# Performance work log

Measured on AMD Instinct MI355X. Metric: run time of the kernel, lower is better.

The kernel has to match this reference:

```python
import jax, jax.numpy as jnp
import numpy as np

# Stochastic-computing layer: values in [0,1] are encoded as random bitstreams
# (bit = uniform <= value), multiply = AND, and the reduction over input rows is
# a chained random MUX (tf.where with p=0.5 coins), then mean over the bit axis.
BATCH, D_IN, D_OUT, BIT_SIZE = 512, 1024, 1024, 128


def setup_inputs() -> dict:
    key = jax.random.key(0)
    kx, kw = jax.random.split(key)
    # bitstream-encoded probabilities in [0, 1]
    x = jax.random.uniform(kx, (BATCH, D_IN), dtype=jnp.float32)
    w = jax.random.uniform(kw, (D_IN, D_OUT), dtype=jnp.float32)
    return {"x": x, "w": w}


def reference(x, w):
    B, Din = x.shape
    Dout = w.shape[1]
    key = jax.random.key(42)
    kx, kw, kc = jax.random.split(key, 3)

    # bitstream generation: bit = (uniform <= value)
    x_bits = jax.random.uniform(kx, (B, Din, BIT_SIZE)) <= x[:, :, None]        # (B, Din, T) bool
    w_bits = jax.random.uniform(kw, (Din, Dout, BIT_SIZE)) <= w[:, :, None]     # (Din, Dout, T) bool

    # Chained random MUX over rows 1..Din-2 (mirrors `for row in range(1, dim-1)`):
    #   final = where(coin, final, row_r)  ->  result is row r of the LAST step
    #   whose coin was False; row 0 if every coin was True. Coins are shared
    #   across the output dim (original select_line shape (B, 1, T)).
    n_steps = Din - 2
    coins = jax.random.uniform(kc, (n_steps, B, BIT_SIZE)) <= 0.5               # (steps, B, T) bool
    rows = jnp.arange(1, Din - 1)                                               # (steps,)
    idx = jnp.max(jnp.where(~coins, rows[:, None, None], 0), axis=0)            # (B, T) int

    # Gather the selected row's bits instead of materializing (B, Din, Dout, T)
    chosen_x = jnp.take_along_axis(x_bits, idx[:, None, :], axis=1)[:, 0, :]    # (B, T)
    w_bt = jnp.transpose(w_bits, (0, 2, 1))                                     # (Din, T, Dout)
    chosen_w = w_bt[idx, jnp.arange(BIT_SIZE)[None, :], :]                      # (B, T, Dout)

    # stochastic multiply (AND) then decode via mean over the bit axis
    final = (chosen_x[:, :, None] & chosen_w).astype(jnp.float32)               # (B, T, Dout)
    return jnp.mean(final, axis=1)                                              # (B, Dout)
```

## Files before the change

kernel.cpp:

```cpp
#include <hip/hip_runtime.h>
#include <stdint.h>

#define BATCH 512
#define D_IN 1024
#define D_OUT 1024
#define BITSZ 128
#define N_STEPS (D_IN - 2)

#define IBASE 960
#define ICAP 64

#define WS_V_OFF 0u
#define WS_V_BYTES (BATCH * BITSZ * 4u)
#define WS_TAB_OFF (WS_V_OFF + WS_V_BYTES)
#define WS_TAB_BYTES (BITSZ * ICAP * 32u * 4u)
#define WS_NEEDED (WS_TAB_OFF + WS_TAB_BYTES)

#define MCAP 128
#define TSTRIDE 132

__host__ __device__ __forceinline__ uint32_t rotl32(uint32_t x, uint32_t d) {
  return (x << d) | (x >> (32u - d));
}

__host__ __device__ __forceinline__ void threefry2x32(uint32_t k0, uint32_t k1,
                                                      uint32_t& x0, uint32_t& x1) {
  const uint32_t k2 = k0 ^ k1 ^ 0x1BD11BDAu;
  x0 += k0; x1 += k1;
#define TFR(r) { x0 += x1; x1 = rotl32(x1, (r)); x1 ^= x0; }
  TFR(13) TFR(15) TFR(26) TFR(6)
  x0 += k1; x1 += k2 + 1u;
  TFR(17) TFR(29) TFR(16) TFR(24)
  x0 += k2; x1 += k0 + 2u;
  TFR(13) TFR(15) TFR(26) TFR(6)
  x0 += k0; x1 += k1 + 3u;
  TFR(17) TFR(29) TFR(16) TFR(24)
  x0 += k1; x1 += k2 + 4u;
  TFR(13) TFR(15) TFR(26) TFR(6)
  x0 += k2; x1 += k0 + 5u;
#undef TFR
}

__device__ __forceinline__ float runif(uint32_t k0, uint32_t k1, uint32_t n) {
  uint32_t x0 = 0u, x1 = n;
  threefry2x32(k0, k1, x0, x1);
  const uint32_t b = x0 ^ x1;
  return __uint_as_float((b >> 9) | 0x3f800000u) - 1.0f;
}

__global__ void __launch_bounds__(256) k_idx(const float* __restrict__ x,
                                             int* __restrict__ v,
                                             uint32_t ck0, uint32_t ck1,
                                             uint32_t xk0, uint32_t xk1) {
  const int tid = blockIdx.x * 256 + threadIdx.x;
  const int b = tid >> 7;
  const int t = tid & 127;

  int idx = 0;
  int s;
  for (s = N_STEPS - 1; s >= 3; s -= 4) {
    const float u0 = runif(ck0, ck1, ((uint32_t)(s)     << 16) + (uint32_t)tid);
    const float u1 = runif(ck0, ck1, ((uint32_t)(s - 1) << 16) + (uint32_t)tid);
    const float u2 = runif(ck0, ck1, ((uint32_t)(s - 2) << 16) + (uint32_t)tid);
    const float u3 = runif(ck0, ck1, ((uint32_t)(s - 3) << 16) + (uint32_t)tid);
    if (u0 > 0.5f) { idx = s + 1; break; }
    if (u1 > 0.5f) { idx = s;     break; }
    if (u2 > 0.5f) { idx = s - 1; break; }
    if (u3 > 0.5f) { idx = s - 2; break; }
  }
  if (idx == 0 && s < 3) {
    const float u0 = runif(ck0, ck1, (1u << 16) + (uint32_t)tid);
    const float u1 = runif(ck0, ck1, (uint32_t)tid);
    if (u0 > 0.5f)      idx = 2;
    else if (u1 > 0.5f) idx = 1;
  }

  const float ux = runif(xk0, xk1,
      ((uint32_t)b << 17) + ((uint32_t)idx << 7) + (uint32_t)t);
  const int xb = (ux <= x[b * D_IN + idx]) ? 1 : 0;
  v[tid] = xb ? idx : -1;
}

__global__ void __launch_bounds__(256) k_tab(const float* __restrict__ w,
                                             const int* __restrict__ v,
                                             uint32_t* __restrict__ tab,
                                             uint32_t wk0, uint32_t wk1) {
  const int t = blockIdx.x >> 2;
  const int q = blockIdx.x & 3;
  const int tid = threadIdx.x;

  __shared__ uint32_t s_bm[2];
  if (tid < 2) s_bm[tid] = 0u;
  __syncthreads();

  unsigned long long m64 = 0;
  {
    const int v0 = v[tid * BITSZ + t];
    const int v1 = v[(tid + 256) * BITSZ + t];
    if (v0 >= IBASE) m64 |= 1ull << (v0 - IBASE);
    if (v1 >= IBASE) m64 |= 1ull << (v1 - IBASE);
  }
  for (int off = 32; off; off >>= 1) m64 |= __shfl_down(m64, off);
  if ((tid & 63) == 0) {
    atomicOr(&s_bm[0], (uint32_t)m64);
    atomicOr(&s_bm[1], (uint32_t)(m64 >> 32));
  }
  __syncthreads();

  unsigned long long bm = (unsigned long long)s_bm[0] |
                          ((unsigned long long)s_bm[1] << 32);
  const int d = q * 256 + tid;
  const int lane = tid & 63;
  const int wbase = (d >> 5) & ~1;
  while (bm) {
    const int j = __builtin_ctzll(bm);
    bm &= bm - 1ull;
    const int i = IBASE + j;
    const float u = runif(wk0, wk1,
        ((uint32_t)i << 17) + ((uint32_t)d << 7) + (uint32_t)t);
    const unsigned long long mb = __ballot(u <= w[i * D_OUT + d]);
    uint32_t* row = tab + (((t << 6) + j) << 5);
    if (lane == 0)  row[wbase]     = (uint32_t)mb;
    if (lane == 32) row[wbase + 1] = (uint32_t)(mb >> 32);
  }
}

__global__ void __launch_bounds__(1024) k_acc(const float* __restrict__ w,
                                              const int* __restrict__ v,
                                              const uint32_t* __restrict__ tab,
                                              float* __restrict__ out,
                                              uint32_t wk0, uint32_t wk1,
                                              int use_tab) {
  const int b = blockIdx.x;
  const int tid = threadIdx.x;

  __shared__ __align__(16) uint32_t s_tab2[32 * TSTRIDE];
  __shared__ int s_list[BITSZ];
  __shared__ int s_wcnt[2];
  __shared__ int s_anyfb;

  if (tid == 0) s_anyfb = use_tab ? 0 : 1;
  __syncthreads();

  unsigned long long mb = 0;
  int code = -1;
  bool act = false;
  if (tid < BITSZ) {
    code = v[b * BITSZ + tid];
    act = code >= 0;
    mb = __ballot(act);
    if ((tid & 63) == 0) s_wcnt[tid >> 6] = __popcll(mb);
  }
  __syncthreads();
  const int m = s_wcnt[0] + s_wcnt[1];
  const int m4 = (m + 3) & ~3;
  if (tid < BITSZ && act) {
    const int lane = tid & 63;
    const int pos = ((tid >= 64) ? s_wcnt[0] : 0) +
                    __popcll(mb & ((1ull << lane) - 1ull));
    s_list[pos] = (code << 7) | tid;
    if (code < IBASE) atomicOr(&s_anyfb, 1);
  }
  __syncthreads();

  if (s_anyfb == 0) {
    const int wrd = tid & 31;
    for (int jj = tid >> 5; jj < m; jj += 32) {
      const int e = s_list[jj];
      const int i = e >> 7, t = e & 127;
      s_tab2[wrd * TSTRIDE + jj] = tab[(((t << 6) + (i - IBASE)) << 5) + wrd];
    }
    if (tid < 32)
      for (int jj = m; jj < m4; ++jj) s_tab2[tid * TSTRIDE + jj] = 0u;
    __syncthreads();

    const int dw = tid >> 5, db = tid & 31;
    const uint32_t* colp = &s_tab2[dw * TSTRIDE];
    int acc = 0;
    for (int k = 0; k < m4; k += 4) {
      const uint4 r = *(const uint4*)(colp + k);
      acc += (r.x >> db) & 1u;
      acc += (r.y >> db) & 1u;
      acc += (r.z >> db) & 1u;
      acc += (r.w >> db) & 1u;
    }
    out[b * D_OUT + tid] = (float)acc * (1.0f / (float)BITSZ);
  } else {
    int acc = 0;
    for (int jj = 0; jj < m; ++jj) {
      const int e = s_list[jj];
      const int i = e >> 7, t = e & 127;
      const float u = runif(wk0, wk1,
          ((uint32_t)i << 17) + ((uint32_t)tid << 7) + (uint32_t)t);
      acc += (u <= w[i * D_OUT + tid]) ? 1 : 0;
    }
    out[b * D_OUT + tid] = (float)acc * (1.0f / (float)BITSZ);
  }
}

struct TFKeys { uint32_t xk0, xk1, wk0, wk1, ck0, ck1; };

static TFKeys derive_keys() {
  TFKeys K;
  uint32_t a0 = 0, a1 = 0; threefry2x32(0u, 42u, a0, a1); K.xk0 = a0; K.xk1 = a1;
  uint32_t b0 = 0, b1 = 1; threefry2x32(0u, 42u, b0, b1); K.wk0 = b0; K.wk1 = b1;
  uint32_t c0 = 0, c1 = 2; threefry2x32(0u, 42u, c0, c1); K.ck0 = c0; K.ck1 = c1;
  return K;
}

extern "C" void kernel_launch(void* const* d_in, const int* in_sizes, int n_in,
                              void* d_out, int out_size, void* d_ws, size_t ws_size,
                              hipStream_t stream) {
  const float* x = (const float*)d_in[0];
  const float* w = (const float*)d_in[1];
  if (n_in >= 2 && in_sizes[0] == D_IN * D_OUT && in_sizes[1] == BATCH * D_IN) {
    const float* tmp = x; x = w; w = tmp;
  }
  float* out = (float*)d_out;
  char* ws = (char*)d_ws;
  int* v = (int*)(ws + WS_V_OFF);
  uint32_t* tab = (uint32_t*)(ws + WS_TAB_OFF);

  const int use_tab = (ws_size >= WS_NEEDED) ? 1 : 0;
  const TFKeys K = derive_keys();

  hipLaunchKernelGGL(k_idx, dim3((BATCH * BITSZ) / 256), dim3(256), 0, stream,
                     x, v, K.ck0, K.ck1, K.xk0, K.xk1);
  if (use_tab)
    hipLaunchKernelGGL(k_tab, dim3(BITSZ * 4), dim3(256), 0, stream,
                       w, v, tab, K.wk0, K.wk1);
  hipLaunchKernelGGL(k_acc, dim3(BATCH), dim3(D_OUT), 0, stream,
                     w, v, tab, out, K.wk0, K.wk1, use_tab);
}
```

Baseline: 22.47 us.

## Fuse index scan into table-building kernel to drop one launch

Merges the index-selection kernel and the w-bit table kernel into one. Each of the four output-quarter blocks for a bit position recomputes the coin scan for all 512 batch rows, and only quarter 0 writes v. This removes a kernel launch and the global round trip of v between them, at the cost of doing the Threefry scan work four times. A __syncthreads in k_acc after initialising s_anyfb is also removed; this looks safe because a later barrier comes before the atomicOr on s_anyfb.

```diff
diff --git a/kernel.cpp b/kernel.cpp
--- a/kernel.cpp
+++ b/kernel.cpp
@@ -16,7 +16,6 @@
 #define WS_TAB_BYTES (BITSZ * ICAP * 32u * 4u)
 #define WS_NEEDED (WS_TAB_OFF + WS_TAB_BYTES)
 
-#define MCAP 128
 #define TSTRIDE 132
 
 __host__ __device__ __forceinline__ uint32_t rotl32(uint32_t x, uint32_t d) {
@@ -48,6 +47,79 @@
   return __uint_as_float((b >> 9) | 0x3f800000u) - 1.0f;
 }
 
+__device__ __forceinline__ int scan_idx(int b, int t,
+                                        uint32_t ck0, uint32_t ck1) {
+  const uint32_t bt = ((uint32_t)b << 7) + (uint32_t)t;
+  int idx = 0;
+  int s;
+  for (s = N_STEPS - 1; s >= 3; s -= 4) {
+    const float u0 = runif(ck0, ck1, ((uint32_t)(s)     << 16) + bt);
+    const float u1 = runif(ck0, ck1, ((uint32_t)(s - 1) << 16) + bt);
+    const float u2 = runif(ck0, ck1, ((uint32_t)(s - 2) << 16) + bt);
+    const float u3 = runif(ck0, ck1, ((uint32_t)(s - 3) << 16) + bt);
+    if (u0 > 0.5f) { idx = s + 1; break; }
+    if (u1 > 0.5f) { idx = s;     break; }
+    if (u2 > 0.5f) { idx = s - 1; break; }
+    if (u3 > 0.5f) { idx = s - 2; break; }
+  }
+  if (idx == 0 && s < 3) {
+    const float u0 = runif(ck0, ck1, (1u << 16) + bt);
+    const float u1 = runif(ck0, ck1, bt);
+    if (u0 > 0.5f)      idx = 2;
+    else if (u1 > 0.5f) idx = 1;
+  }
+  return idx;
+}
+
+__global__ void __launch_bounds__(256) k_tabx(const float* __restrict__ x,
+                                              const float* __restrict__ w,
+                                              int* __restrict__ v,
+                                              uint32_t* __restrict__ tab,
+                                              uint32_t ck0, uint32_t ck1,
+                                              uint32_t xk0, uint32_t xk1,
+                                              uint32_t wk0, uint32_t wk1) {
+  const int t = blockIdx.x & 127;
+  const int q = blockIdx.x >> 7;
+  const int tid = threadIdx.x;
+
+  __shared__ uint32_t s_bm[2];
+  if (tid < 2) s_bm[tid] = 0u;
+  __syncthreads();
+
+#pragma unroll
+  for (int h = 0; h < 2; ++h) {
+    const int b = tid + h * 256;
+    const int idx = scan_idx(b, t, ck0, ck1);
+    const float ux = runif(xk0, xk1,
+        ((uint32_t)b << 17) + ((uint32_t)idx << 7) + (uint32_t)t);
+    const int xb = (ux <= x[b * D_IN + idx]) ? 1 : 0;
+    if (q == 0) v[b * BITSZ + t] = xb ? idx : -1;
+    if (xb && idx >= IBASE) {
+      const int bp = idx - IBASE;
+      atomicOr(&s_bm[bp >> 5], 1u << (bp & 31));
+    }
+  }
+  __syncthreads();
+
+  unsigned long long bm = (unsigned long long)s_bm[0] |
+                          ((unsigned long long)s_bm[1] << 32);
+  const int d = q * 256 + tid;
+  const int lane = tid & 63;
+  const int wbase = (d >> 5) & ~1;
+  const float* wcol = w + d;
+  while (bm) {
+    const int j = __builtin_ctzll(bm);
+    bm &= bm - 1ull;
+    const int i = IBASE + j;
+    const float u = runif(wk0, wk1,
+        ((uint32_t)i << 17) + ((uint32_t)d << 7) + (uint32_t)t);
+    const unsigned long long mb = __ballot(u <= wcol[i * D_OUT]);
+    uint32_t* row = tab + (((t << 6) + j) << 5);
+    if (lane == 0)  row[wbase]     = (uint32_t)mb;
+    if (lane == 32) row[wbase + 1] = (uint32_t)(mb >> 32);
+  }
+}
+
 __global__ void __launch_bounds__(256) k_idx(const float* __restrict__ x,
                                              int* __restrict__ v,
                                              uint32_t ck0, uint32_t ck1,
@@ -55,74 +127,11 @@
   const int tid = blockIdx.x * 256 + threadIdx.x;
   const int b = tid >> 7;
   const int t = tid & 127;
-
-  int idx = 0;
-  int s;
-  for (s = N_STEPS - 1; s >= 3; s -= 4) {
-    const float u0 = runif(ck0, ck1, ((uint32_t)(s)     << 16) + (uint32_t)tid);
-    const float u1 = runif(ck0, ck1, ((uint32_t)(s - 1) << 16) + (uint32_t)tid);
-    const float u2 = runif(ck0, ck1, ((uint32_t)(s - 2) << 16) + (uint32_t)tid);
-    const float u3 = runif(ck0, ck1, ((uint32_t)(s - 3) << 16) + (uint32_t)tid);
-    if (u0 > 0.5f) { idx = s + 1; break; }
-    if (u1 > 0.5f) { idx = s;     break; }
-    if (u2 > 0.5f) { idx = s - 1; break; }
-    if (u3 > 0.5f) { idx = s - 2; break; }
-  }
-  if (idx == 0 && s < 3) {
-    const float u0 = runif(ck0, ck1, (1u << 16) + (uint32_t)tid);
-    const float u1 = runif(ck0, ck1, (uint32_t)tid);
-    if (u0 > 0.5f)      idx = 2;
-    else if (u1 > 0.5f) idx = 1;
-  }
-
+  const int idx = scan_idx(b, t, ck0, ck1);
   const float ux = runif(xk0, xk1,
       ((uint32_t)b << 17) + ((uint32_t)idx << 7) + (uint32_t)t);
   const int xb = (ux <= x[b * D_IN + idx]) ? 1 : 0;
   v[tid] = xb ? idx : -1;
-}
-
-__global__ void __launch_bounds__(256) k_tab(const float* __restrict__ w,
-                                             const int* __restrict__ v,
-                                             uint32_t* __restrict__ tab,
-                                             uint32_t wk0, uint32_t wk1) {
-  const int t = blockIdx.x >> 2;
-  const int q = blockIdx.x & 3;
-  const int tid = threadIdx.x;
-
-  __shared__ uint32_t s_bm[2];
-  if (tid < 2) s_bm[tid] = 0u;
-  __syncthreads();
-
-  unsigned long long m64 = 0;
-  {
-    const int v0 = v[tid * BITSZ + t];
-    const int v1 = v[(tid + 256) * BITSZ + t];
-    if (v0 >= IBASE) m64 |= 1ull << (v0 - IBASE);
-    if (v1 >= IBASE) m64 |= 1ull << (v1 - IBASE);
-  }
-  for (int off = 32; off; off >>= 1) m64 |= __shfl_down(m64, off);
-  if ((tid & 63) == 0) {
-    atomicOr(&s_bm[0], (uint32_t)m64);
-    atomicOr(&s_bm[1], (uint32_t)(m64 >> 32));
-  }
-  __syncthreads();
-
-  unsigned long long bm = (unsigned long long)s_bm[0] |
-                          ((unsigned long long)s_bm[1] << 32);
-  const int d = q * 256 + tid;
-  const int lane = tid & 63;
-  const int wbase = (d >> 5) & ~1;
-  while (bm) {
-    const int j = __builtin_ctzll(bm);
-    bm &= bm - 1ull;
-    const int i = IBASE + j;
-    const float u = runif(wk0, wk1,
-        ((uint32_t)i << 17) + ((uint32_t)d << 7) + (uint32_t)t);
-    const unsigned long long mb = __ballot(u <= w[i * D_OUT + d]);
-    uint32_t* row = tab + (((t << 6) + j) << 5);
-    if (lane == 0)  row[wbase]     = (uint32_t)mb;
-    if (lane == 32) row[wbase + 1] = (uint32_t)(mb >> 32);
-  }
 }
 
 __global__ void __launch_bounds__(1024) k_acc(const float* __restrict__ w,
@@ -140,7 +149,6 @@
   __shared__ int s_anyfb;
 
   if (tid == 0) s_anyfb = use_tab ? 0 : 1;
-  __syncthreads();
 
   unsigned long long mb = 0;
   int code = -1;
@@ -224,11 +232,13 @@
   const int use_tab = (ws_size >= WS_NEEDED) ? 1 : 0;
   const TFKeys K = derive_keys();
 
-  hipLaunchKernelGGL(k_idx, dim3((BATCH * BITSZ) / 256), dim3(256), 0, stream,
-                     x, v, K.ck0, K.ck1, K.xk0, K.xk1);
-  if (use_tab)
-    hipLaunchKernelGGL(k_tab, dim3(BITSZ * 4), dim3(256), 0, stream,
-                       w, v, tab, K.wk0, K.wk1);
+  if (use_tab) {
+    hipLaunchKernelGGL(k_tabx, dim3(BITSZ * 4), dim3(256), 0, stream,
+                       x, w, v, tab, K.ck0, K.ck1, K.xk0, K.xk1, K.wk0, K.wk1);
+  } else {
+    hipLaunchKernelGGL(k_idx, dim3((BATCH * BITSZ) / 256), dim3(256), 0, stream,
+                       x, v, K.ck0, K.ck1, K.xk0, K.xk1);
+  }
   hipLaunchKernelGGL(k_acc, dim3(BATCH), dim3(D_OUT), 0, stream,
                      w, v, tab, out, K.wk0, K.wk1, use_tab);
 }
```

Measured after the change: 25.14 us. 1.12x slower.
